# Kernel optimization log

Hardware: AMD Instinct MI355X
Metric: run time of the kernel (lower is better)

Reference implementation:

```python
import jax, jax.numpy as jnp
import numpy as np

SOS_TOKEN = 0


def setup_inputs() -> dict:
    key = jax.random.key(0)
    ks = jax.random.split(key, 16)
    B, S, T, H, V = 64, 64, 32, 512, 32000
    s = 1.0 / np.sqrt(H)
    inp = {
        "encoder_outputs": jax.random.normal(ks[0], (B, S, H), jnp.float32),
        "encoder_hidden": jax.random.normal(ks[1], (1, B, H), jnp.float32),
        "target_tensor": jax.random.randint(ks[2], (B, T), 0, V),
        "emb": jax.random.normal(ks[3], (V, H), jnp.float32),
        "Wa": jax.random.uniform(ks[4], (H, H), jnp.float32, -s, s),
        "ba": jnp.zeros((H,), jnp.float32),
        "Ua": jax.random.uniform(ks[5], (H, H), jnp.float32, -s, s),
        "bu": jnp.zeros((H,), jnp.float32),
        "va": jax.random.uniform(ks[6], (H, 1), jnp.float32, -s, s),
        "bv": jnp.zeros((1,), jnp.float32),
        "w_ih": jax.random.uniform(ks[7], (3 * H, 2 * H), jnp.float32, -s, s),
        "b_ih": jax.random.uniform(ks[8], (3 * H,), jnp.float32, -s, s),
        "w_hh": jax.random.uniform(ks[9], (3 * H, H), jnp.float32, -s, s),
        "b_hh": jax.random.uniform(ks[10], (3 * H,), jnp.float32, -s, s),
        "Wo": jax.random.uniform(ks[11], (V, H), jnp.float32, -s, s),
        "bo": jax.random.uniform(ks[12], (V,), jnp.float32, -s, s),
    }
    return inp


def _gru_cell(x, h, w_ih, b_ih, w_hh, b_hh):
    # x: [B, 2H], h: [B, H] -- PyTorch nn.GRU gate math
    H = h.shape[-1]
    gi = x @ w_ih.T + b_ih            # [B, 3H]
    gh = h @ w_hh.T + b_hh            # [B, 3H]
    i_r, i_z, i_n = gi[:, :H], gi[:, H:2 * H], gi[:, 2 * H:]
    h_r, h_z, h_n = gh[:, :H], gh[:, H:2 * H], gh[:, 2 * H:]
    r = jax.nn.sigmoid(i_r + h_r)
    z = jax.nn.sigmoid(i_z + h_z)
    n = jnp.tanh(i_n + r * h_n)
    return (1.0 - z) * n + z * h


def reference(encoder_outputs, encoder_hidden, target_tensor,
              emb, Wa, ba, Ua, bu, va, bv,
              w_ih, b_ih, w_hh, b_hh, Wo, bo):
    B, S, H = encoder_outputs.shape
    T = target_tensor.shape[1]
    # Teacher forcing: step t input is SOS for t=0 else target[:, t-1]
    sos = jnp.full((B, 1), SOS_TOKEN, dtype=target_tensor.dtype)
    input_ids = jnp.concatenate([sos, target_tensor[:, :-1]], axis=1)  # [B, T]
    embedded = emb[input_ids]  # [B, T, H]  (dropout is identity in eval)

    # Precompute key projection once (invariant across steps)
    Ua_keys = encoder_outputs @ Ua.T + bu  # [B, S, H]

    def step(h, x_emb):
        # Bahdanau additive attention: query = hidden state
        scores = jnp.tanh(h[:, None, :] @ Wa.T + ba + Ua_keys) @ va + bv  # [B, S, 1]
        scores = scores[..., 0]                                           # [B, S]
        attn = jax.nn.softmax(scores, axis=-1)
        context = jnp.einsum('bs,bsh->bh', attn, encoder_outputs)
        x = jnp.concatenate([x_emb, context], axis=-1)                    # [B, 2H]
        h_new = _gru_cell(x, h, w_ih, b_ih, w_hh, b_hh)
        logits = h_new @ Wo.T + bo                                        # [B, V]
        return h_new, (logits, attn)

    h0 = encoder_hidden[0]  # [B, H]
    h_final, (logits_t, attn_t) = jax.lax.scan(step, h0, jnp.swapaxes(embedded, 0, 1))
    logits = jnp.swapaxes(logits_t, 0, 1)        # [B, T, V]
    attentions = jnp.swapaxes(attn_t, 0, 1)      # [B, T, S]
    log_probs = jax.nn.log_softmax(logits, axis=-1)
    decoder_hidden = h_final[None]               # [1, B, H]
    return (log_probs, decoder_hidden, attentions)
```

## Files before the change

kernel.cpp:

```cpp
#include <hip/hip_runtime.h>

typedef unsigned short u16;
typedef __bf16 bf16x8 __attribute__((ext_vector_type(8)));
typedef float f32x4 __attribute__((ext_vector_type(4)));

#define Bsz 64
#define Ssz 64
#define Tsz 32
#define Hsz 512
#define Vsz 32000
#define NCONV 160
#define NTOT 256

#define MAIL_BG 0
#define MAIL_GB 2048
#define MAIL_GG 4096
#define NMAIL 5120

static __device__ inline u16 f2bf(float f) {
    union { float f; unsigned u; } v; v.f = f;
    unsigned u = v.u;
    unsigned r = (u + 0x7FFFu + ((u >> 16) & 1u)) >> 16;
    return (u16)r;
}
static __device__ inline float bf2f(u16 v) {
    union { unsigned u; float f; } x; x.u = ((unsigned)v) << 16; return x.f;
}
static __device__ inline float tanh_fast(float x) {
    float e = __expf(2.f * x);
    return 1.f - 2.f / (e + 1.f);
}
static __device__ inline void st_u32(unsigned* p, unsigned v) {
    __hip_atomic_store(p, v, __ATOMIC_RELAXED, __HIP_MEMORY_SCOPE_AGENT);
}
static __device__ inline unsigned ld_u32(const unsigned* p) {
    return __hip_atomic_load(p, __ATOMIC_RELAXED, __HIP_MEMORY_SCOPE_AGENT);
}

#define GLOAD_LDS16(g, l) \
    __builtin_amdgcn_global_load_lds((const __attribute__((address_space(1))) void*)(g), \
                                     (__attribute__((address_space(3))) void*)(l), 16, 0, 0)

__global__ void prep_kernel(const float* __restrict__ enc, const float* __restrict__ Ua,
                            const float* __restrict__ Wa, const float* __restrict__ wih,
                            const float* __restrict__ whh, const float* __restrict__ ehid,
                            const int* __restrict__ target, const float* __restrict__ emb,
                            u16* __restrict__ encbf, u16* __restrict__ Uabf,
                            u16* __restrict__ Wabf, u16* __restrict__ wihbf,
                            u16* __restrict__ whhbf, u16* __restrict__ h0bf,
                            u16* __restrict__ xbuf) {
    const int n0 = 2097152, n1 = 262144, n2 = 262144, n3 = 1572864, n4 = 786432, n5 = 32768;
    const int n6 = Tsz * Bsz * Hsz;
    const int total = n0 + n1 + n2 + n3 + n4 + n5 + n6;
    for (int i = blockIdx.x * blockDim.x + threadIdx.x; i < total; i += gridDim.x * blockDim.x) {
        int j = i;
        if (j < n0) { encbf[j] = f2bf(enc[j]); continue; } j -= n0;
        if (j < n1) { Uabf[j] = f2bf(Ua[j]); continue; } j -= n1;
        if (j < n2) { Wabf[j] = f2bf(Wa[j]); continue; } j -= n2;
        if (j < n3) { wihbf[j] = f2bf(wih[j]); continue; } j -= n3;
        if (j < n4) { whhbf[j] = f2bf(whh[j]); continue; } j -= n4;
        if (j < n5) { h0bf[j] = f2bf(ehid[j]); continue; } j -= n5;
        {
            int t = j / (Bsz * Hsz);
            int rem = j % (Bsz * Hsz);
            int b = rem / Hsz, k = rem % Hsz;
            int id = (t == 0) ? 0 : target[b * Tsz + (t - 1)];
            xbuf[((size_t)t * Bsz + b) * 1024 + k] = f2bf(emb[(size_t)id * Hsz + k]);
        }
    }
}

__global__ __launch_bounds__(256) void gemm_bt(const u16* __restrict__ A, const u16* __restrict__ Bw,
                                               const float* __restrict__ bias, float* __restrict__ out,
                                               int M, int N, int K) {
    __shared__ __align__(16) u16 As[128 * 32];
    __shared__ __align__(16) u16 Bs[128 * 32];
    int m0 = blockIdx.x * 128, n0 = blockIdx.y * 128;
    int tid = threadIdx.x, lane = tid & 63, wid = tid >> 6;
    int wm = wid & 1, wn = wid >> 1;
    f32x4 acc[4][4] = {};
    for (int k0 = 0; k0 < K; k0 += 32) {
        int e0 = wid * 64 + lane;
        int e1 = e0 + 256;
        GLOAD_LDS16(&A[(size_t)(m0 + (e0 >> 2)) * K + k0 + (e0 & 3) * 8], (char*)As + wid * 1024);
        GLOAD_LDS16(&A[(size_t)(m0 + (e1 >> 2)) * K + k0 + (e1 & 3) * 8], (char*)As + 4096 + wid * 1024);
        GLOAD_LDS16(&Bw[(size_t)(n0 + (e0 >> 2)) * K + k0 + (e0 & 3) * 8], (char*)Bs + wid * 1024);
        GLOAD_LDS16(&Bw[(size_t)(n0 + (e1 >> 2)) * K + k0 + (e1 & 3) * 8], (char*)Bs + 4096 + wid * 1024);
        __syncthreads();
        bf16x8 av[4], bvv[4];
        for (int mi = 0; mi < 4; ++mi)
            av[mi] = *(const bf16x8*)&As[(wm * 64 + mi * 16 + (lane & 15)) * 32 + (lane >> 4) * 8];
        for (int ni = 0; ni < 4; ++ni)
            bvv[ni] = *(const bf16x8*)&Bs[(wn * 64 + ni * 16 + (lane & 15)) * 32 + (lane >> 4) * 8];
        for (int mi = 0; mi < 4; ++mi)
            for (int ni = 0; ni < 4; ++ni)
                acc[mi][ni] = __builtin_amdgcn_mfma_f32_16x16x32_bf16(av[mi], bvv[ni], acc[mi][ni], 0, 0, 0);
        __syncthreads();
    }
    for (int mi = 0; mi < 4; ++mi)
        for (int ni = 0; ni < 4; ++ni) {
            int n = n0 + wn * 64 + ni * 16 + (lane & 15);
            float bb = bias[n];
            for (int r = 0; r < 4; ++r) {
                int m = m0 + wm * 64 + mi * 16 + (lane >> 4) * 4 + r;
                out[(size_t)m * N + n] = acc[mi][ni][r] + bb;
            }
        }
}

__global__ __launch_bounds__(512, 1) void coop_kernel(
    const float* __restrict__ uak,
    u16* __restrict__ xbuf, u16* __restrict__ Abf,
    const u16* __restrict__ h0bf, const u16* __restrict__ wihbf, const u16* __restrict__ whhbf,
    const u16* __restrict__ Wabf, const float* __restrict__ enc,
    const float* __restrict__ va, const float* __restrict__ bv, const float* __restrict__ ba,
    const float* __restrict__ b_ih, const float* __restrict__ b_hh,
    const float* __restrict__ ehid,
    const float* __restrict__ Wo, u16* __restrict__ Wobf,
    float* __restrict__ out, u16* __restrict__ partials,
    unsigned* __restrict__ bar) {
    __shared__ __align__(16) char lds[149504];
    __shared__ float WhL[512];
    __shared__ float scL[64];
    __shared__ float vaL[512];

    const size_t HID_OFF = (size_t)Bsz * Tsz * Vsz;
    const size_t ATT_OFF = HID_OFF + (size_t)Bsz * Hsz;

    int tid = threadIdx.x, lane = tid & 63, wid = tid >> 6;
    int ln15 = lane & 15, hi = lane >> 4;
    int bx = blockIdx.x;

    unsigned* xbufU = (unsigned*)xbuf;
    unsigned* AbfU = (unsigned*)Abf;
    unsigned* partU = (unsigned*)partials;

    if (bx < 64) {
        int b = bx;
        u16* uakL = (u16*)lds;
        u16* encL = (u16*)(lds + 65536);
        float* attL = (float*)(lds + 131072);
        for (int i = tid; i < Ssz * Hsz; i += 512) {
            uakL[i] = f2bf(uak[(size_t)b * Ssz * Hsz + i]);
            encL[i] = f2bf(enc[(size_t)b * Ssz * Hsz + i]);
        }
        vaL[tid] = va[tid];
        float bvv = bv[0];
        float ba_t = ba[tid];
        int halfsel = tid & 1;
        __syncthreads();

        for (int t = 0; t < Tsz; ++t) {
            if (tid < 32) {
                unsigned* p = &bar[(MAIL_GB + b * 32 + tid) * 32];
                while (ld_u32(p) < (unsigned)(t + 1)) asm volatile("s_sleep 1");
            }
            __syncthreads();
            {
                float acc = ba_t;
                const unsigned* pb = partU + (size_t)b * 256 + (tid >> 1);
#pragma unroll
                for (int g = 0; g < 32; ++g) {
                    unsigned pw = ld_u32(pb + (size_t)g * 16384);
                    acc += bf2f((u16)(halfsel ? (pw >> 16) : (pw & 0xffff)));
                }
                WhL[tid] = acc;
            }
            __syncthreads();
            for (int si = 0; si < 8; ++si) {
                int s = wid * 8 + si;
                float a = 0.f;
#pragma unroll
                for (int ji = 0; ji < 8; ++ji) {
                    int j = lane + ji * 64;
                    float x = WhL[j] + bf2f(uakL[s * 512 + j]);
                    a += tanh_fast(x) * vaL[j];
                }
                for (int off = 32; off; off >>= 1) a += __shfl_down(a, off);
                if (lane == 0) scL[s] = a + bvv;
            }
            __syncthreads();
            if (wid == 0) {
                float x = scL[lane];
                float mx = x;
                for (int off = 32; off; off >>= 1) mx = fmaxf(mx, __shfl_xor(mx, off));
                float e = __expf(x - mx);
                float sm = e;
                for (int off = 32; off; off >>= 1) sm += __shfl_xor(sm, off);
                float at = e / sm;
                scL[lane] = at;
                attL[t * 64 + lane] = at;
            }
            __syncthreads();
            float c = 0.f;
            for (int s = 0; s < Ssz; ++s)
                c += scL[s] * bf2f(encL[s * 512 + tid]);
            unsigned me = (unsigned)f2bf(c);
            unsigned other = __shfl_xor(me, 1);
            if ((tid & 1) == 0)
                st_u32(&xbufU[((size_t)t * Bsz + b) * 512 + 256 + (tid >> 1)], me | (other << 16));
            asm volatile("s_waitcnt vmcnt(0)" ::: "memory");
            __syncthreads();
            if (tid < 32) st_u32(&bar[(MAIL_BG + tid * 64 + b) * 32], (unsigned)(t + 1));
        }
        __syncthreads();
        for (int i = tid; i < Tsz * Ssz; i += 512)
            out[ATT_OFF + (size_t)b * (Tsz * Ssz) + i] = attL[i];
    } else if (bx < 96) {
        int g = bx - 64, jbase = g * 16;
        u16* hsl = (u16*)(lds + 147456);
        for (int i = tid; i < 6144; i += 512) {
            int row = i >> 7, c16 = i & 127;
            int Rg = (row >> 4) * 512 + jbase + (row & 15);
            uint4 v = *(const uint4*)&wihbf[(size_t)Rg * 1024 + c16 * 8];
            *(uint4*)(lds + row * 2048 + ((c16 * 16) ^ ((row & 7) << 4))) = v;
        }
        for (int i = tid; i < 3072; i += 512) {
            int row = i >> 6, c16 = i & 63;
            int Rg = (row >> 4) * 512 + jbase + (row & 15);
            uint4 v = *(const uint4*)&whhbf[(size_t)Rg * 512 + c16 * 8];
            *(uint4*)(lds + 98304 + row * 1024 + ((c16 * 16) ^ ((row & 7) << 4))) = v;
        }
        const char* wih_l = lds;
        const char* whh_l = lds + 98304;
        int j = jbase + ln15;
        float bir = b_ih[j] + b_hh[j];
        float biz = b_ih[512 + j] + b_hh[512 + j];
        float bin = b_ih[1024 + j];
        float bhn = b_hh[1024 + j];
        float hp0 = 0.f, hp1 = 0.f, hp2 = 0.f, hp3 = 0.f;
        if (wid < 4) {
            int m = wid;
            hp0 = ehid[(size_t)(m * 16 + hi * 4 + 0) * Hsz + j];
            hp1 = ehid[(size_t)(m * 16 + hi * 4 + 1) * Hsz + j];
            hp2 = ehid[(size_t)(m * 16 + hi * 4 + 2) * Hsz + j];
            hp3 = ehid[(size_t)(m * 16 + hi * 4 + 3) * Hsz + j];
        }
        int swz = (ln15 & 7) << 4;
        bf16x8 zfr = {};
        bf16x8 wfrag[4];
#pragma unroll
        for (int i = 0; i < 4; ++i) {
            int jp = (wid * 4 + i) * 16 + ln15;
            wfrag[i] = (hi < 2) ? *(const bf16x8*)&Wabf[(size_t)jp * 512 + jbase + hi * 8] : zfr;
        }
        for (int i = tid; i < 1024; i += 512)
            hsl[i] = h0bf[(size_t)(i >> 4) * 512 + jbase + (i & 15)];
        __syncthreads();
#pragma unroll
        for (int mt = 0; mt < 4; ++mt) {
            bf16x8 af = (hi < 2) ? *(const bf16x8*)&hsl[(mt * 16 + ln15) * 16 + hi * 8] : zfr;
#pragma unroll
            for (int i = 0; i < 4; ++i) {
                f32x4 pacc = {};
                pacc = __builtin_amdgcn_mfma_f32_16x16x32_bf16(af, wfrag[i], pacc, 0, 0, 0);
                int n0 = (wid * 4 + i) * 16;
#pragma unroll
                for (int r = 0; r < 4; ++r) {
                    int b = mt * 16 + hi * 4 + r;
                    unsigned me = (unsigned)f2bf(pacc[r]);
                    unsigned other = __shfl_xor(me, 1);
                    if ((ln15 & 1) == 0)
                        st_u32(&partU[((size_t)g * 64 + b) * 256 + ((n0 + ln15) >> 1)], me | (other << 16));
                }
            }
        }
        asm volatile("s_waitcnt vmcnt(0)" ::: "memory");
        __syncthreads();
        if (tid < 64) st_u32(&bar[(MAIL_GB + tid * 32 + g) * 32], 1u);
        else if (tid < 96) st_u32(&bar[(MAIL_GG + (tid - 64) * 32 + g) * 32], 1u);

        for (int t = 0; t < Tsz; ++t) {
            const u16* hbt = t ? (Abf + (size_t)(t - 1) * Bsz * Hsz) : h0bf;
            f32x4 ar = {}, az = {}, ain = {}, ahn = {};
            if (wid < 4) {
                int m = wid;
#pragma unroll 8
                for (int k0 = 0; k0 < 16; ++k0) {
                    bf16x8 a = *(const bf16x8*)&xbuf[((size_t)t * Bsz + m * 16 + ln15) * 1024 + k0 * 32 + hi * 8];
                    int byteIn = k0 * 64 + hi * 16;
                    bf16x8 b0 = *(const bf16x8*)(wih_l + (0 + ln15) * 2048 + (byteIn ^ swz));
                    bf16x8 b1 = *(const bf16x8*)(wih_l + (16 + ln15) * 2048 + (byteIn ^ swz));
                    bf16x8 b2 = *(const bf16x8*)(wih_l + (32 + ln15) * 2048 + (byteIn ^ swz));
                    ar = __builtin_amdgcn_mfma_f32_16x16x32_bf16(a, b0, ar, 0, 0, 0);
                    az = __builtin_amdgcn_mfma_f32_16x16x32_bf16(a, b1, az, 0, 0, 0);
                    ain = __builtin_amdgcn_mfma_f32_16x16x32_bf16(a, b2, ain, 0, 0, 0);
                }
            }
            if (tid < 32) {
                unsigned* p = &bar[(MAIL_GG + g * 32 + tid) * 32];
                while (ld_u32(p) < (unsigned)(t + 1)) asm volatile("s_sleep 1");
            }
            __syncthreads();
            if (wid < 4) {
                int m = wid;
#pragma unroll 8
                for (int k0 = 0; k0 < 16; ++k0) {
                    bf16x8 a = *(const bf16x8*)&hbt[(size_t)(m * 16 + ln15) * 512 + k0 * 32 + hi * 8];
                    int byteIn = k0 * 64 + hi * 16;
                    bf16x8 b0 = *(const bf16x8*)(whh_l + (0 + ln15) * 1024 + (byteIn ^ swz));
                    bf16x8 b1 = *(const bf16x8*)(whh_l + (16 + ln15) * 1024 + (byteIn ^ swz));
                    bf16x8 b2 = *(const bf16x8*)(whh_l + (32 + ln15) * 1024 + (byteIn ^ swz));
                    ar = __builtin_amdgcn_mfma_f32_16x16x32_bf16(a, b0, ar, 0, 0, 0);
                    az = __builtin_amdgcn_mfma_f32_16x16x32_bf16(a, b1, az, 0, 0, 0);
                    ahn = __builtin_amdgcn_mfma_f32_16x16x32_bf16(a, b2, ahn, 0, 0, 0);
                }
                unsigned* p = &bar[(MAIL_BG + g * 64 + wid * 16 + ln15) * 32];
                while (ld_u32(p) < (unsigned)(t + 1)) asm volatile("s_sleep 1");
#pragma unroll 8
                for (int k0 = 16; k0 < 32; ++k0) {
                    bf16x8 a = *(const bf16x8*)&xbuf[((size_t)t * Bsz + m * 16 + ln15) * 1024 + k0 * 32 + hi * 8];
                    int byteIn = k0 * 64 + hi * 16;
                    bf16x8 b0 = *(const bf16x8*)(wih_l + (0 + ln15) * 2048 + (byteIn ^ swz));
                    bf16x8 b1 = *(const bf16x8*)(wih_l + (16 + ln15) * 2048 + (byteIn ^ swz));
                    bf16x8 b2 = *(const bf16x8*)(wih_l + (32 + ln15) * 2048 + (byteIn ^ swz));
                    ar = __builtin_amdgcn_mfma_f32_16x16x32_bf16(a, b0, ar, 0, 0, 0);
                    az = __builtin_amdgcn_mfma_f32_16x16x32_bf16(a, b1, az, 0, 0, 0);
                    ain = __builtin_amdgcn_mfma_f32_16x16x32_bf16(a, b2, ain, 0, 0, 0);
                }
                float hpv[4] = {hp0, hp1, hp2, hp3};
#pragma unroll
                for (int r = 0; r < 4; ++r) {
                    int b = m * 16 + hi * 4 + r;
                    float rg = 1.f / (1.f + __expf(-(ar[r] + bir)));
                    float zg = 1.f / (1.f + __expf(-(az[r] + biz)));
                    float ng = tanh_fast(ain[r] + bin + rg * (ahn[r] + bhn));
                    float hv = (1.f - zg) * ng + zg * hpv[r];
                    hpv[r] = hv;
                    u16 hb = f2bf(hv);
                    unsigned me = (unsigned)hb;
                    unsigned other = __shfl_xor(me, 1);
                    if ((ln15 & 1) == 0)
                        st_u32(&AbfU[((size_t)t * Bsz + b) * 256 + (j >> 1)], me | (other << 16));
                    hsl[b * 16 + ln15] = hb;
                    if (t == Tsz - 1) out[HID_OFF + (size_t)b * 512 + j] = hv;
                }
                hp0 = hpv[0]; hp1 = hpv[1]; hp2 = hpv[2]; hp3 = hpv[3];
            }
            __syncthreads();
#pragma unroll
            for (int mt = 0; mt < 4; ++mt) {
                bf16x8 af = (hi < 2) ? *(const bf16x8*)&hsl[(mt * 16 + ln15) * 16 + hi * 8] : zfr;
#pragma unroll
                for (int i = 0; i < 4; ++i) {
                    f32x4 pacc = {};
                    pacc = __builtin_amdgcn_mfma_f32_16x16x32_bf16(af, wfrag[i], pacc, 0, 0, 0);
                    int n0 = (wid * 4 + i) * 16;
#pragma unroll
                    for (int r = 0; r < 4; ++r) {
                        int b = mt * 16 + hi * 4 + r;
                        unsigned me = (unsigned)f2bf(pacc[r]);
                        unsigned other = __shfl_xor(me, 1);
                        if ((ln15 & 1) == 0)
                            st_u32(&partU[((size_t)g * 64 + b) * 256 + ((n0 + ln15) >> 1)], me | (other << 16));
                    }
                }
            }
            asm volatile("s_waitcnt vmcnt(0)" ::: "memory");
            __syncthreads();
            if (tid < 64) st_u32(&bar[(MAIL_GB + tid * 32 + g) * 32], (unsigned)(t + 2));
            else if (tid < 96) st_u32(&bar[(MAIL_GG + (tid - 64) * 32 + g) * 32], (unsigned)(t + 2));
        }
    } else {
        const float4* W4 = (const float4*)Wo;
        for (int i = (bx - 96) * 512 + tid; i < (Vsz * Hsz) / 4; i += NCONV * 512) {
            float4 v = W4[i];
            ushort4 o;
            o.x = f2bf(v.x); o.y = f2bf(v.y); o.z = f2bf(v.z); o.w = f2bf(v.w);
            *(ushort4*)&Wobf[(size_t)i * 4] = o;
        }
    }
}

template <int BF16OUT>
__global__ __launch_bounds__(512) void gemm_logits(const u16* __restrict__ Abf, const u16* __restrict__ Wobf,
                                                   const float* __restrict__ bo, float* __restrict__ out,
                                                   u16* __restrict__ scr, float* __restrict__ sumexp) {
    __shared__ __align__(16) char lds[49152];
    char* As0 = lds;
    char* Bs0 = lds + 8192;
    char* As1 = lds + 24576;
    char* Bs1 = lds + 32768;
    int tid = threadIdx.x, lane = tid & 63, wid = tid >> 6;
    int ln15 = lane & 15, hi = lane >> 4;
    int wm = wid & 1, wn = wid >> 1;
    int job = blockIdx.x;
    int m0 = (job / 125) * 128, n0 = (job % 125) * 256;
    f32x4 acc[4][4] = {};
    {
        int e0 = wid * 64 + lane, r = e0 >> 2, c8 = (e0 & 3) * 8;
        GLOAD_LDS16(&Abf[(size_t)(m0 + r) * 512 + c8], As0 + wid * 1024);
        GLOAD_LDS16(&Wobf[(size_t)(n0 + r) * 512 + c8], Bs0 + wid * 1024);
        GLOAD_LDS16(&Wobf[(size_t)(n0 + 128 + r) * 512 + c8], Bs0 + 8192 + wid * 1024);
    }
#pragma unroll 2
    for (int ks = 0; ks < 16; ++ks) {
        const u16* As = (const u16*)((ks & 1) ? As1 : As0);
        const u16* Bs = (const u16*)((ks & 1) ? Bs1 : Bs0);
        if (ks < 15) {
            char* Asn = (ks & 1) ? As0 : As1;
            char* Bsn = (ks & 1) ? Bs0 : Bs1;
            int e0 = wid * 64 + lane, r = e0 >> 2, c8 = (e0 & 3) * 8;
            int k0 = (ks + 1) * 32;
            GLOAD_LDS16(&Abf[(size_t)(m0 + r) * 512 + k0 + c8], Asn + wid * 1024);
            GLOAD_LDS16(&Wobf[(size_t)(n0 + r) * 512 + k0 + c8], Bsn + wid * 1024);
            GLOAD_LDS16(&Wobf[(size_t)(n0 + 128 + r) * 512 + k0 + c8], Bsn + 8192 + wid * 1024);
            asm volatile("s_waitcnt vmcnt(3)" ::: "memory");
        } else {
            asm volatile("s_waitcnt vmcnt(0)" ::: "memory");
        }
        __builtin_amdgcn_s_barrier();
        bf16x8 av[4], bvv[4];
        for (int mi = 0; mi < 4; ++mi)
            av[mi] = *(const bf16x8*)&As[(wm * 64 + mi * 16 + ln15) * 32 + hi * 8];
        for (int ni = 0; ni < 4; ++ni)
            bvv[ni] = *(const bf16x8*)&Bs[(wn * 64 + ni * 16 + ln15) * 32 + hi * 8];
        for (int mi = 0; mi < 4; ++mi)
            for (int ni = 0; ni < 4; ++ni)
                acc[mi][ni] = __builtin_amdgcn_mfma_f32_16x16x32_bf16(av[mi], bvv[ni], acc[mi][ni], 0, 0, 0);
        asm volatile("s_waitcnt lgkmcnt(0)" ::: "memory");
        __builtin_amdgcn_s_barrier();
    }
    float* eps = (float*)lds;
    float bb[4];
#pragma unroll
    for (int ni = 0; ni < 4; ++ni) bb[ni] = bo[n0 + wn * 64 + ni * 16 + ln15];
    for (int mi = 0; mi < 4; ++mi) {
        __syncthreads();
#pragma unroll
        for (int ni = 0; ni < 4; ++ni)
#pragma unroll
            for (int r = 0; r < 4; ++r)
                eps[(wm * 16 + hi * 4 + r) * 256 + wn * 64 + ni * 16 + ln15] = acc[mi][ni][r] + bb[ni];
        __syncthreads();
#pragma unroll
        for (int k = 0; k < 4; ++k) {
            int idx = k * 512 + tid;
            int l = idx >> 6, c4 = idx & 63;
            int m = m0 + (l >> 4) * 64 + mi * 16 + (l & 15);
            int t = m >> 6, b = m & 63;
            float4 v = *(float4*)&eps[l * 256 + c4 * 4];
            if (BF16OUT) {
                ushort4 o;
                o.x = f2bf(v.x); o.y = f2bf(v.y); o.z = f2bf(v.z); o.w = f2bf(v.w);
                *(ushort4*)&scr[((size_t)(b * Tsz + t)) * Vsz + n0 + c4 * 4] = o;
            } else {
                *(float4*)&out[((size_t)(b * Tsz + t)) * Vsz + n0 + c4 * 4] = v;
            }
            float e = __expf(v.x) + __expf(v.y) + __expf(v.z) + __expf(v.w);
            for (int off = 32; off; off >>= 1) e += __shfl_down(e, off);
            if (lane == 0) atomicAdd(&sumexp[(m & 63) * Tsz + (m >> 6)], e);
        }
    }
}

__global__ void sub_kernel(float* __restrict__ out, const float* __restrict__ sumexp) {
    const int total4 = (Bsz * Tsz * Vsz) / 4;
    float4* o4 = (float4*)out;
    for (int i = blockIdx.x * blockDim.x + threadIdx.x; i < total4; i += gridDim.x * blockDim.x) {
        float l = __logf(sumexp[i / (Vsz / 4)]);
        float4 v = o4[i];
        v.x -= l; v.y -= l; v.z -= l; v.w -= l;
        o4[i] = v;
    }
}

__global__ void sub_bf16_kernel(const u16* __restrict__ scr, const float* __restrict__ sumexp,
                                float* __restrict__ out) {
    const int total8 = (Bsz * Tsz * Vsz) / 8;
    for (int i = blockIdx.x * blockDim.x + threadIdx.x; i < total8; i += gridDim.x * blockDim.x) {
        float l = __logf(sumexp[i / (Vsz / 8)]);
        uint4 v = *(const uint4*)&scr[(size_t)i * 8];
        float4 a, b;
        a.x = bf2f((u16)v.x) - l;        a.y = bf2f((u16)(v.x >> 16)) - l;
        a.z = bf2f((u16)v.y) - l;        a.w = bf2f((u16)(v.y >> 16)) - l;
        b.x = bf2f((u16)v.z) - l;        b.y = bf2f((u16)(v.z >> 16)) - l;
        b.z = bf2f((u16)v.w) - l;        b.w = bf2f((u16)(v.w >> 16)) - l;
        *(float4*)&out[(size_t)i * 8] = a;
        *(float4*)&out[(size_t)i * 8 + 4] = b;
    }
}

extern "C" void kernel_launch(void* const* d_in, const int* in_sizes, int n_in,
                              void* d_out, int out_size, void* d_ws, size_t ws_size,
                              hipStream_t stream) {
    const float* enc   = (const float*)d_in[0];
    const float* ehid  = (const float*)d_in[1];
    const int*   target= (const int*)d_in[2];
    const float* emb   = (const float*)d_in[3];
    const float* Wa    = (const float*)d_in[4];
    const float* ba    = (const float*)d_in[5];
    const float* Ua    = (const float*)d_in[6];
    const float* bu    = (const float*)d_in[7];
    const float* va    = (const float*)d_in[8];
    const float* bv    = (const float*)d_in[9];
    const float* w_ih  = (const float*)d_in[10];
    const float* b_ih  = (const float*)d_in[11];
    const float* w_hh  = (const float*)d_in[12];
    const float* b_hh  = (const float*)d_in[13];
    const float* Wo    = (const float*)d_in[14];
    const float* bo    = (const float*)d_in[15];
    float* out = (float*)d_out;

    char* w = (char*)d_ws;
    float* uak    = (float*)w; w += (size_t)4096 * 512 * 4;
    float* sumexp = (float*)w; w += 8192;
    unsigned* bar = (unsigned*)w; w += (size_t)NMAIL * 128;
    u16* xbuf     = (u16*)w;   w += (size_t)Tsz * Bsz * 1024 * 2;
    u16* Abf      = (u16*)w;   w += (size_t)Tsz * Bsz * Hsz * 2;
    u16* h0bf     = (u16*)w;   w += (size_t)Bsz * Hsz * 2;
    u16* partials = (u16*)w;   w += (size_t)32 * Bsz * Hsz * 2;
    u16* Wabf     = (u16*)w;   w += (size_t)Hsz * Hsz * 2;
    u16* encbf    = (u16*)w;   w += (size_t)4096 * 512 * 2;
    u16* Uabf     = (u16*)w;   w += (size_t)Hsz * Hsz * 2;
    u16* wihbf    = (u16*)w;   w += (size_t)1536 * 1024 * 2;
    u16* whhbf    = (u16*)w;   w += (size_t)1536 * 512 * 2;
    u16* Wobf     = (u16*)w;   w += (size_t)Vsz * 512 * 2;
    u16* scrbf    = (u16*)w;   w += (size_t)Bsz * Tsz * Vsz * 2;
    const int use_bf16 = (ws_size >= (size_t)(w - (char*)d_ws));

    prep_kernel<<<2048, 256, 0, stream>>>(enc, Ua, Wa, w_ih, w_hh, ehid, target, emb,
                                          encbf, Uabf, Wabf, wihbf, whhbf, h0bf, xbuf);

    gemm_bt<<<dim3(32, 4), 256, 0, stream>>>(encbf, Uabf, bu, uak, 4096, 512, 512);

    hipMemsetAsync(bar, 0, (size_t)NMAIL * 128, stream);
    hipMemsetAsync(sumexp, 0, 2048 * 4, stream);

    coop_kernel<<<NTOT, 512, 0, stream>>>(uak, xbuf, Abf, h0bf, wihbf, whhbf,
                                          Wabf, enc, va, bv, ba, b_ih, b_hh,
                                          ehid, Wo, Wobf, out, partials, bar);

    if (use_bf16) {
        gemm_logits<1><<<2000, 512, 0, stream>>>(Abf, Wobf, bo, out, scrbf, sumexp);
        sub_bf16_kernel<<<4096, 256, 0, stream>>>(scrbf, sumexp, out);
    } else {
        gemm_logits<0><<<2000, 512, 0, stream>>>(Abf, Wobf, bo, out, scrbf, sumexp);
        sub_kernel<<<2048, 256, 0, stream>>>(out, sumexp);
    }
}
```

Baseline: 819.3 us.

## Fuse key projection GEMM and weight bf16 conversion into cooperative kernel

Removes the separate gemm_bt launch and fp32 uak round trip by computing the Ua key projection per batch inside the attention blocks with MFMA from LDS-resident encoder data. The GRU blocks now convert w_ih/w_hh from fp32 to bf16 while loading into LDS, so the prep kernel no longer converts encoder outputs or GRU weights. This cuts launches and global traffic but adds serial work at the start of the persistent kernel, reading Ua fragments straight from global memory.

Result: no change. 819.7 us (+0.1%).

```diff
diff --git a/kernel.cpp b/kernel.cpp
--- a/kernel.cpp
+++ b/kernel.cpp
@@ -36,29 +36,31 @@
 static __device__ inline unsigned ld_u32(const unsigned* p) {
     return __hip_atomic_load(p, __ATOMIC_RELAXED, __HIP_MEMORY_SCOPE_AGENT);
 }
+static __device__ inline uint4 pack8(float4 a, float4 b) {
+    uint4 o;
+    o.x = (unsigned)f2bf(a.x) | ((unsigned)f2bf(a.y) << 16);
+    o.y = (unsigned)f2bf(a.z) | ((unsigned)f2bf(a.w) << 16);
+    o.z = (unsigned)f2bf(b.x) | ((unsigned)f2bf(b.y) << 16);
+    o.w = (unsigned)f2bf(b.z) | ((unsigned)f2bf(b.w) << 16);
+    return o;
+}
 
 #define GLOAD_LDS16(g, l) \
     __builtin_amdgcn_global_load_lds((const __attribute__((address_space(1))) void*)(g), \
                                      (__attribute__((address_space(3))) void*)(l), 16, 0, 0)
 
-__global__ void prep_kernel(const float* __restrict__ enc, const float* __restrict__ Ua,
-                            const float* __restrict__ Wa, const float* __restrict__ wih,
-                            const float* __restrict__ whh, const float* __restrict__ ehid,
+__global__ void prep_kernel(const float* __restrict__ Ua, const float* __restrict__ Wa,
+                            const float* __restrict__ ehid,
                             const int* __restrict__ target, const float* __restrict__ emb,
-                            u16* __restrict__ encbf, u16* __restrict__ Uabf,
-                            u16* __restrict__ Wabf, u16* __restrict__ wihbf,
-                            u16* __restrict__ whhbf, u16* __restrict__ h0bf,
-                            u16* __restrict__ xbuf) {
-    const int n0 = 2097152, n1 = 262144, n2 = 262144, n3 = 1572864, n4 = 786432, n5 = 32768;
+                            u16* __restrict__ Uabf, u16* __restrict__ Wabf,
+                            u16* __restrict__ h0bf, u16* __restrict__ xbuf) {
+    const int n1 = 262144, n2 = 262144, n5 = 32768;
     const int n6 = Tsz * Bsz * Hsz;
-    const int total = n0 + n1 + n2 + n3 + n4 + n5 + n6;
+    const int total = n1 + n2 + n5 + n6;
     for (int i = blockIdx.x * blockDim.x + threadIdx.x; i < total; i += gridDim.x * blockDim.x) {
         int j = i;
-        if (j < n0) { encbf[j] = f2bf(enc[j]); continue; } j -= n0;
         if (j < n1) { Uabf[j] = f2bf(Ua[j]); continue; } j -= n1;
         if (j < n2) { Wabf[j] = f2bf(Wa[j]); continue; } j -= n2;
-        if (j < n3) { wihbf[j] = f2bf(wih[j]); continue; } j -= n3;
-        if (j < n4) { whhbf[j] = f2bf(whh[j]); continue; } j -= n4;
         if (j < n5) { h0bf[j] = f2bf(ehid[j]); continue; } j -= n5;
         {
             int t = j / (Bsz * Hsz);
@@ -70,48 +72,10 @@
     }
 }
 
-__global__ __launch_bounds__(256) void gemm_bt(const u16* __restrict__ A, const u16* __restrict__ Bw,
-                                               const float* __restrict__ bias, float* __restrict__ out,
-                                               int M, int N, int K) {
-    __shared__ __align__(16) u16 As[128 * 32];
-    __shared__ __align__(16) u16 Bs[128 * 32];
-    int m0 = blockIdx.x * 128, n0 = blockIdx.y * 128;
-    int tid = threadIdx.x, lane = tid & 63, wid = tid >> 6;
-    int wm = wid & 1, wn = wid >> 1;
-    f32x4 acc[4][4] = {};
-    for (int k0 = 0; k0 < K; k0 += 32) {
-        int e0 = wid * 64 + lane;
-        int e1 = e0 + 256;
-        GLOAD_LDS16(&A[(size_t)(m0 + (e0 >> 2)) * K + k0 + (e0 & 3) * 8], (char*)As + wid * 1024);
-        GLOAD_LDS16(&A[(size_t)(m0 + (e1 >> 2)) * K + k0 + (e1 & 3) * 8], (char*)As + 4096 + wid * 1024);
-        GLOAD_LDS16(&Bw[(size_t)(n0 + (e0 >> 2)) * K + k0 + (e0 & 3) * 8], (char*)Bs + wid * 1024);
-        GLOAD_LDS16(&Bw[(size_t)(n0 + (e1 >> 2)) * K + k0 + (e1 & 3) * 8], (char*)Bs + 4096 + wid * 1024);
-        __syncthreads();
-        bf16x8 av[4], bvv[4];
-        for (int mi = 0; mi < 4; ++mi)
-            av[mi] = *(const bf16x8*)&As[(wm * 64 + mi * 16 + (lane & 15)) * 32 + (lane >> 4) * 8];
-        for (int ni = 0; ni < 4; ++ni)
-            bvv[ni] = *(const bf16x8*)&Bs[(wn * 64 + ni * 16 + (lane & 15)) * 32 + (lane >> 4) * 8];
-        for (int mi = 0; mi < 4; ++mi)
-            for (int ni = 0; ni < 4; ++ni)
-                acc[mi][ni] = __builtin_amdgcn_mfma_f32_16x16x32_bf16(av[mi], bvv[ni], acc[mi][ni], 0, 0, 0);
-        __syncthreads();
-    }
-    for (int mi = 0; mi < 4; ++mi)
-        for (int ni = 0; ni < 4; ++ni) {
-            int n = n0 + wn * 64 + ni * 16 + (lane & 15);
-            float bb = bias[n];
-            for (int r = 0; r < 4; ++r) {
-                int m = m0 + wm * 64 + mi * 16 + (lane >> 4) * 4 + r;
-                out[(size_t)m * N + n] = acc[mi][ni][r] + bb;
-            }
-        }
-}
-
 __global__ __launch_bounds__(512, 1) void coop_kernel(
-    const float* __restrict__ uak,
     u16* __restrict__ xbuf, u16* __restrict__ Abf,
-    const u16* __restrict__ h0bf, const u16* __restrict__ wihbf, const u16* __restrict__ whhbf,
+    const u16* __restrict__ h0bf, const u16* __restrict__ Uabf, const float* __restrict__ bu,
+    const float* __restrict__ wih, const float* __restrict__ whh,
     const u16* __restrict__ Wabf, const float* __restrict__ enc,
     const float* __restrict__ va, const float* __restrict__ bv, const float* __restrict__ ba,
     const float* __restrict__ b_ih, const float* __restrict__ b_hh,
@@ -140,14 +104,41 @@
         u16* uakL = (u16*)lds;
         u16* encL = (u16*)(lds + 65536);
         float* attL = (float*)(lds + 131072);
-        for (int i = tid; i < Ssz * Hsz; i += 512) {
-            uakL[i] = f2bf(uak[(size_t)b * Ssz * Hsz + i]);
+        for (int i = tid; i < Ssz * Hsz; i += 512)
             encL[i] = f2bf(enc[(size_t)b * Ssz * Hsz + i]);
-        }
         vaL[tid] = va[tid];
         float bvv = bv[0];
         float ba_t = ba[tid];
         int halfsel = tid & 1;
+        __syncthreads();
+        {
+            f32x4 ua[4][4] = {};
+#pragma unroll
+            for (int k0 = 0; k0 < 16; ++k0) {
+                bf16x8 af[4], bfr[4];
+#pragma unroll
+                for (int mt = 0; mt < 4; ++mt)
+                    af[mt] = *(const bf16x8*)&encL[(mt * 16 + ln15) * 512 + k0 * 32 + hi * 8];
+#pragma unroll
+                for (int jt = 0; jt < 4; ++jt)
+                    bfr[jt] = *(const bf16x8*)&Uabf[(size_t)(wid * 64 + jt * 16 + ln15) * 512 + k0 * 32 + hi * 8];
+#pragma unroll
+                for (int mt = 0; mt < 4; ++mt)
+#pragma unroll
+                    for (int jt = 0; jt < 4; ++jt)
+                        ua[mt][jt] = __builtin_amdgcn_mfma_f32_16x16x32_bf16(af[mt], bfr[jt], ua[mt][jt], 0, 0, 0);
+            }
+#pragma unroll
+            for (int mt = 0; mt < 4; ++mt)
+#pragma unroll
+                for (int jt = 0; jt < 4; ++jt) {
+                    int jj = wid * 64 + jt * 16 + ln15;
+                    float bj = bu[jj];
+#pragma unroll
+                    for (int r = 0; r < 4; ++r)
+                        uakL[(mt * 16 + hi * 4 + r) * 512 + jj] = f2bf(ua[mt][jt][r] + bj);
+                }
+        }
         __syncthreads();
 
         for (int t = 0; t < Tsz; ++t) {
@@ -212,14 +203,18 @@
         for (int i = tid; i < 6144; i += 512) {
             int row = i >> 7, c16 = i & 127;
             int Rg = (row >> 4) * 512 + jbase + (row & 15);
-            uint4 v = *(const uint4*)&wihbf[(size_t)Rg * 1024 + c16 * 8];
-            *(uint4*)(lds + row * 2048 + ((c16 * 16) ^ ((row & 7) << 4))) = v;
+            const float* src = &wih[(size_t)Rg * 1024 + c16 * 8];
+            float4 v0 = *(const float4*)src;
+            float4 v1 = *(const float4*)(src + 4);
+            *(uint4*)(lds + row * 2048 + ((c16 * 16) ^ ((row & 7) << 4))) = pack8(v0, v1);
         }
         for (int i = tid; i < 3072; i += 512) {
             int row = i >> 6, c16 = i & 63;
             int Rg = (row >> 4) * 512 + jbase + (row & 15);
-            uint4 v = *(const uint4*)&whhbf[(size_t)Rg * 512 + c16 * 8];
-            *(uint4*)(lds + 98304 + row * 1024 + ((c16 * 16) ^ ((row & 7) << 4))) = v;
+            const float* src = &whh[(size_t)Rg * 512 + c16 * 8];
+            float4 v0 = *(const float4*)src;
+            float4 v1 = *(const float4*)(src + 4);
+            *(uint4*)(lds + 98304 + row * 1024 + ((c16 * 16) ^ ((row & 7) << 4))) = pack8(v0, v1);
         }
         const char* wih_l = lds;
         const char* whh_l = lds + 98304;
@@ -503,7 +498,6 @@
     float* out = (float*)d_out;
 
     char* w = (char*)d_ws;
-    float* uak    = (float*)w; w += (size_t)4096 * 512 * 4;
     float* sumexp = (float*)w; w += 8192;
     unsigned* bar = (unsigned*)w; w += (size_t)NMAIL * 128;
     u16* xbuf     = (u16*)w;   w += (size_t)Tsz * Bsz * 1024 * 2;
@@ -511,23 +505,17 @@
     u16* h0bf     = (u16*)w;   w += (size_t)Bsz * Hsz * 2;
     u16* partials = (u16*)w;   w += (size_t)32 * Bsz * Hsz * 2;
     u16* Wabf     = (u16*)w;   w += (size_t)Hsz * Hsz * 2;
-    u16* encbf    = (u16*)w;   w += (size_t)4096 * 512 * 2;
     u16* Uabf     = (u16*)w;   w += (size_t)Hsz * Hsz * 2;
-    u16* wihbf    = (u16*)w;   w += (size_t)1536 * 1024 * 2;
-    u16* whhbf    = (u16*)w;   w += (size_t)1536 * 512 * 2;
     u16* Wobf     = (u16*)w;   w += (size_t)Vsz * 512 * 2;
     u16* scrbf    = (u16*)w;   w += (size_t)Bsz * Tsz * Vsz * 2;
     const int use_bf16 = (ws_size >= (size_t)(w - (char*)d_ws));
 
-    prep_kernel<<<2048, 256, 0, stream>>>(enc, Ua, Wa, w_ih, w_hh, ehid, target, emb,
-                                          encbf, Uabf, Wabf, wihbf, whhbf, h0bf, xbuf);
-
-    gemm_bt<<<dim3(32, 4), 256, 0, stream>>>(encbf, Uabf, bu, uak, 4096, 512, 512);
+    prep_kernel<<<512, 256, 0, stream>>>(Ua, Wa, ehid, target, emb, Uabf, Wabf, h0bf, xbuf);
 
     hipMemsetAsync(bar, 0, (size_t)NMAIL * 128, stream);
     hipMemsetAsync(sumexp, 0, 2048 * 4, stream);
 
-    coop_kernel<<<NTOT, 512, 0, stream>>>(uak, xbuf, Abf, h0bf, wihbf, whhbf,
+    coop_kernel<<<NTOT, 512, 0, stream>>>(xbuf, Abf, h0bf, Uabf, bu, w_ih, w_hh,
                                           Wabf, enc, va, bv, ba, b_ih, b_hh,
                                           ehid, Wo, Wobf, out, partials, bar);
 
```

## Compute full query projection in dedicated waves and simplify mailbox synchronisation

Applied to the files above, without the earlier changes.

The old code had GRU blocks compute 16-wide K-slices of h@Wa.T and write 32 partial sums, which attention blocks then reduced. Now waves 4-7 of each GRU block compute full-K output tiles of h@Wa.T for their 16 columns, reading h from global memory. They write one bf16 result per step and signal per-wave flags, so attention blocks do a single load instead of a 32-way reduction. GRU waves no longer need a block-wide barrier and signal per wave; wih/whh are converted to bf16 inside the coop kernel instead of in prep. The cost is a longer query-projection step (16 MFMAs over the full K) sitting on the critical path of the recurrence, plus per-step global reads of h.

Measured after the change: 835.3 us. Within noise of the previous version (+2.0%).

```diff
diff --git a/kernel.cpp b/kernel.cpp
--- a/kernel.cpp
+++ b/kernel.cpp
@@ -12,10 +12,9 @@
 #define NCONV 160
 #define NTOT 256
 
-#define MAIL_BG 0
-#define MAIL_GB 2048
-#define MAIL_GG 4096
-#define NMAIL 5120
+#define FW_BASE 128
+#define FC_BASE 256
+#define NSLOT 320
 
 static __device__ inline u16 f2bf(float f) {
     union { float f; unsigned u; } v; v.f = f;
@@ -36,29 +35,33 @@
 static __device__ inline unsigned ld_u32(const unsigned* p) {
     return __hip_atomic_load(p, __ATOMIC_RELAXED, __HIP_MEMORY_SCOPE_AGENT);
 }
+static __device__ inline uint4 pack8(float4 a, float4 b) {
+    uint4 o;
+    o.x = (unsigned)f2bf(a.x) | ((unsigned)f2bf(a.y) << 16);
+    o.y = (unsigned)f2bf(a.z) | ((unsigned)f2bf(a.w) << 16);
+    o.z = (unsigned)f2bf(b.x) | ((unsigned)f2bf(b.y) << 16);
+    o.w = (unsigned)f2bf(b.z) | ((unsigned)f2bf(b.w) << 16);
+    return o;
+}
 
 #define GLOAD_LDS16(g, l) \
     __builtin_amdgcn_global_load_lds((const __attribute__((address_space(1))) void*)(g), \
                                      (__attribute__((address_space(3))) void*)(l), 16, 0, 0)
 
 __global__ void prep_kernel(const float* __restrict__ enc, const float* __restrict__ Ua,
-                            const float* __restrict__ Wa, const float* __restrict__ wih,
-                            const float* __restrict__ whh, const float* __restrict__ ehid,
+                            const float* __restrict__ Wa, const float* __restrict__ ehid,
                             const int* __restrict__ target, const float* __restrict__ emb,
                             u16* __restrict__ encbf, u16* __restrict__ Uabf,
-                            u16* __restrict__ Wabf, u16* __restrict__ wihbf,
-                            u16* __restrict__ whhbf, u16* __restrict__ h0bf,
+                            u16* __restrict__ Wabf, u16* __restrict__ h0bf,
                             u16* __restrict__ xbuf) {
-    const int n0 = 2097152, n1 = 262144, n2 = 262144, n3 = 1572864, n4 = 786432, n5 = 32768;
+    const int n0 = 2097152, n1 = 262144, n2 = 262144, n5 = 32768;
     const int n6 = Tsz * Bsz * Hsz;
-    const int total = n0 + n1 + n2 + n3 + n4 + n5 + n6;
+    const int total = n0 + n1 + n2 + n5 + n6;
     for (int i = blockIdx.x * blockDim.x + threadIdx.x; i < total; i += gridDim.x * blockDim.x) {
         int j = i;
         if (j < n0) { encbf[j] = f2bf(enc[j]); continue; } j -= n0;
         if (j < n1) { Uabf[j] = f2bf(Ua[j]); continue; } j -= n1;
         if (j < n2) { Wabf[j] = f2bf(Wa[j]); continue; } j -= n2;
-        if (j < n3) { wihbf[j] = f2bf(wih[j]); continue; } j -= n3;
-        if (j < n4) { whhbf[j] = f2bf(whh[j]); continue; } j -= n4;
         if (j < n5) { h0bf[j] = f2bf(ehid[j]); continue; } j -= n5;
         {
             int t = j / (Bsz * Hsz);
@@ -111,15 +114,16 @@
 __global__ __launch_bounds__(512, 1) void coop_kernel(
     const float* __restrict__ uak,
     u16* __restrict__ xbuf, u16* __restrict__ Abf,
-    const u16* __restrict__ h0bf, const u16* __restrict__ wihbf, const u16* __restrict__ whhbf,
+    const u16* __restrict__ h0bf,
+    const float* __restrict__ wih, const float* __restrict__ whh,
     const u16* __restrict__ Wabf, const float* __restrict__ enc,
     const float* __restrict__ va, const float* __restrict__ bv, const float* __restrict__ ba,
     const float* __restrict__ b_ih, const float* __restrict__ b_hh,
     const float* __restrict__ ehid,
     const float* __restrict__ Wo, u16* __restrict__ Wobf,
-    float* __restrict__ out, u16* __restrict__ partials,
+    float* __restrict__ out, unsigned* __restrict__ WhbU,
     unsigned* __restrict__ bar) {
-    __shared__ __align__(16) char lds[149504];
+    __shared__ __align__(16) char lds[147456];
     __shared__ float WhL[512];
     __shared__ float scL[64];
     __shared__ float vaL[512];
@@ -133,10 +137,10 @@
 
     unsigned* xbufU = (unsigned*)xbuf;
     unsigned* AbfU = (unsigned*)Abf;
-    unsigned* partU = (unsigned*)partials;
 
     if (bx < 64) {
         int b = bx;
+        int mtile = b >> 4;
         u16* uakL = (u16*)lds;
         u16* encL = (u16*)(lds + 65536);
         float* attL = (float*)(lds + 131072);
@@ -152,19 +156,13 @@
 
         for (int t = 0; t < Tsz; ++t) {
             if (tid < 32) {
-                unsigned* p = &bar[(MAIL_GB + b * 32 + tid) * 32];
+                unsigned* p = &bar[(FW_BASE + tid * 4 + mtile) * 32];
                 while (ld_u32(p) < (unsigned)(t + 1)) asm volatile("s_sleep 1");
             }
             __syncthreads();
             {
-                float acc = ba_t;
-                const unsigned* pb = partU + (size_t)b * 256 + (tid >> 1);
-#pragma unroll
-                for (int g = 0; g < 32; ++g) {
-                    unsigned pw = ld_u32(pb + (size_t)g * 16384);
-                    acc += bf2f((u16)(halfsel ? (pw >> 16) : (pw & 0xffff)));
-                }
-                WhL[tid] = acc;
+                unsigned pw = ld_u32(&WhbU[(size_t)t * 16384 + b * 256 + (tid >> 1)]);
+                WhL[tid] = bf2f((u16)(halfsel ? (pw >> 16) : (pw & 0xffff))) + ba_t;
             }
             __syncthreads();
             for (int si = 0; si < 8; ++si) {
@@ -201,80 +199,78 @@
                 st_u32(&xbufU[((size_t)t * Bsz + b) * 512 + 256 + (tid >> 1)], me | (other << 16));
             asm volatile("s_waitcnt vmcnt(0)" ::: "memory");
             __syncthreads();
-            if (tid < 32) st_u32(&bar[(MAIL_BG + tid * 64 + b) * 32], (unsigned)(t + 1));
+            if (tid == 0) st_u32(&bar[(FC_BASE + b) * 32], (unsigned)(t + 1));
         }
         __syncthreads();
         for (int i = tid; i < Tsz * Ssz; i += 512)
             out[ATT_OFF + (size_t)b * (Tsz * Ssz) + i] = attL[i];
     } else if (bx < 96) {
         int g = bx - 64, jbase = g * 16;
-        u16* hsl = (u16*)(lds + 147456);
         for (int i = tid; i < 6144; i += 512) {
             int row = i >> 7, c16 = i & 127;
             int Rg = (row >> 4) * 512 + jbase + (row & 15);
-            uint4 v = *(const uint4*)&wihbf[(size_t)Rg * 1024 + c16 * 8];
-            *(uint4*)(lds + row * 2048 + ((c16 * 16) ^ ((row & 7) << 4))) = v;
+            const float* src = &wih[(size_t)Rg * 1024 + c16 * 8];
+            float4 v0 = *(const float4*)src;
+            float4 v1 = *(const float4*)(src + 4);
+            *(uint4*)(lds + row * 2048 + ((c16 * 16) ^ ((row & 7) << 4))) = pack8(v0, v1);
         }
         for (int i = tid; i < 3072; i += 512) {
             int row = i >> 6, c16 = i & 63;
             int Rg = (row >> 4) * 512 + jbase + (row & 15);
-            uint4 v = *(const uint4*)&whhbf[(size_t)Rg * 512 + c16 * 8];
-            *(uint4*)(lds + 98304 + row * 1024 + ((c16 * 16) ^ ((row & 7) << 4))) = v;
-        }
-        const char* wih_l = lds;
-        const char* whh_l = lds + 98304;
-        int j = jbase + ln15;
-        float bir = b_ih[j] + b_hh[j];
-        float biz = b_ih[512 + j] + b_hh[512 + j];
-        float bin = b_ih[1024 + j];
-        float bhn = b_hh[1024 + j];
-        float hp0 = 0.f, hp1 = 0.f, hp2 = 0.f, hp3 = 0.f;
-        if (wid < 4) {
-            int m = wid;
-            hp0 = ehid[(size_t)(m * 16 + hi * 4 + 0) * Hsz + j];
-            hp1 = ehid[(size_t)(m * 16 + hi * 4 + 1) * Hsz + j];
-            hp2 = ehid[(size_t)(m * 16 + hi * 4 + 2) * Hsz + j];
-            hp3 = ehid[(size_t)(m * 16 + hi * 4 + 3) * Hsz + j];
-        }
-        int swz = (ln15 & 7) << 4;
-        bf16x8 zfr = {};
-        bf16x8 wfrag[4];
-#pragma unroll
-        for (int i = 0; i < 4; ++i) {
-            int jp = (wid * 4 + i) * 16 + ln15;
-            wfrag[i] = (hi < 2) ? *(const bf16x8*)&Wabf[(size_t)jp * 512 + jbase + hi * 8] : zfr;
-        }
-        for (int i = tid; i < 1024; i += 512)
-            hsl[i] = h0bf[(size_t)(i >> 4) * 512 + jbase + (i & 15)];
-        __syncthreads();
-#pragma unroll
-        for (int mt = 0; mt < 4; ++mt) {
-            bf16x8 af = (hi < 2) ? *(const bf16x8*)&hsl[(mt * 16 + ln15) * 16 + hi * 8] : zfr;
-#pragma unroll
-            for (int i = 0; i < 4; ++i) {
-                f32x4 pacc = {};
-                pacc = __builtin_amdgcn_mfma_f32_16x16x32_bf16(af, wfrag[i], pacc, 0, 0, 0);
-                int n0 = (wid * 4 + i) * 16;
+            const float* src = &whh[(size_t)Rg * 512 + c16 * 8];
+            float4 v0 = *(const float4*)src;
+            float4 v1 = *(const float4*)(src + 4);
+            *(uint4*)(lds + 98304 + row * 1024 + ((c16 * 16) ^ ((row & 7) << 4))) = pack8(v0, v1);
+        }
+        __syncthreads();
+
+        if (wid >= 4) {
+            int i = wid - 4;
+            bf16x8 wfragW[16];
+#pragma unroll
+            for (int k0 = 0; k0 < 16; ++k0)
+                wfragW[k0] = *(const bf16x8*)&Wabf[(size_t)(jbase + ln15) * 512 + k0 * 32 + hi * 8];
+            for (int t = 0; t < Tsz; ++t) {
+                const u16* hbt = t ? (Abf + (size_t)(t - 1) * Bsz * Hsz) : h0bf;
+                if (t) {
+                    unsigned* p = &bar[((lane & 31) * 4 + i) * 32];
+                    while (ld_u32(p) < (unsigned)t) asm volatile("s_sleep 1");
+                }
+                f32x4 accW = {};
+#pragma unroll
+                for (int k0 = 0; k0 < 16; ++k0) {
+                    bf16x8 a = *(const bf16x8*)&hbt[(size_t)(i * 16 + ln15) * 512 + k0 * 32 + hi * 8];
+                    accW = __builtin_amdgcn_mfma_f32_16x16x32_bf16(a, wfragW[k0], accW, 0, 0, 0);
+                }
+                unsigned* WhT = WhbU + (size_t)t * 16384;
 #pragma unroll
                 for (int r = 0; r < 4; ++r) {
-                    int b = mt * 16 + hi * 4 + r;
-                    unsigned me = (unsigned)f2bf(pacc[r]);
+                    unsigned me = (unsigned)f2bf(accW[r]);
                     unsigned other = __shfl_xor(me, 1);
                     if ((ln15 & 1) == 0)
-                        st_u32(&partU[((size_t)g * 64 + b) * 256 + ((n0 + ln15) >> 1)], me | (other << 16));
-                }
-            }
-        }
-        asm volatile("s_waitcnt vmcnt(0)" ::: "memory");
-        __syncthreads();
-        if (tid < 64) st_u32(&bar[(MAIL_GB + tid * 32 + g) * 32], 1u);
-        else if (tid < 96) st_u32(&bar[(MAIL_GG + (tid - 64) * 32 + g) * 32], 1u);
-
-        for (int t = 0; t < Tsz; ++t) {
-            const u16* hbt = t ? (Abf + (size_t)(t - 1) * Bsz * Hsz) : h0bf;
-            f32x4 ar = {}, az = {}, ain = {}, ahn = {};
-            if (wid < 4) {
-                int m = wid;
+                        st_u32(&WhT[(i * 16 + hi * 4 + r) * 256 + ((jbase + ln15) >> 1)], me | (other << 16));
+                }
+                asm volatile("s_waitcnt vmcnt(0)" ::: "memory");
+                if (lane == 0) st_u32(&bar[(FW_BASE + g * 4 + i) * 32], (unsigned)(t + 1));
+            }
+        } else {
+            int m = wid;
+            const char* wih_l = lds;
+            const char* whh_l = lds + 98304;
+            int j = jbase + ln15;
+            float bir = b_ih[j] + b_hh[j];
+            float biz = b_ih[512 + j] + b_hh[512 + j];
+            float bin = b_ih[1024 + j];
+            float bhn = b_hh[1024 + j];
+            float hp0 = ehid[(size_t)(m * 16 + hi * 4 + 0) * Hsz + j];
+            float hp1 = ehid[(size_t)(m * 16 + hi * 4 + 1) * Hsz + j];
+            float hp2 = ehid[(size_t)(m * 16 + hi * 4 + 2) * Hsz + j];
+            float hp3 = ehid[(size_t)(m * 16 + hi * 4 + 3) * Hsz + j];
+            int swz = (ln15 & 7) << 4;
+
+            for (int t = 0; t < Tsz; ++t) {
+                const u16* hbt = t ? (Abf + (size_t)(t - 1) * Bsz * Hsz) : h0bf;
+                f32x4 ar = {}, az = {}, ain = {}, ahn = {};
 #pragma unroll 8
                 for (int k0 = 0; k0 < 16; ++k0) {
                     bf16x8 a = *(const bf16x8*)&xbuf[((size_t)t * Bsz + m * 16 + ln15) * 1024 + k0 * 32 + hi * 8];
@@ -286,14 +282,10 @@
                     az = __builtin_amdgcn_mfma_f32_16x16x32_bf16(a, b1, az, 0, 0, 0);
                     ain = __builtin_amdgcn_mfma_f32_16x16x32_bf16(a, b2, ain, 0, 0, 0);
                 }
-            }
-            if (tid < 32) {
-                unsigned* p = &bar[(MAIL_GG + g * 32 + tid) * 32];
-                while (ld_u32(p) < (unsigned)(t + 1)) asm volatile("s_sleep 1");
-            }
-            __syncthreads();
-            if (wid < 4) {
-                int m = wid;
+                if (t) {
+                    unsigned* p = &bar[((lane & 31) * 4 + m) * 32];
+                    while (ld_u32(p) < (unsigned)t) asm volatile("s_sleep 1");
+                }
 #pragma unroll 8
                 for (int k0 = 0; k0 < 16; ++k0) {
                     bf16x8 a = *(const bf16x8*)&hbt[(size_t)(m * 16 + ln15) * 512 + k0 * 32 + hi * 8];
@@ -305,8 +297,10 @@
                     az = __builtin_amdgcn_mfma_f32_16x16x32_bf16(a, b1, az, 0, 0, 0);
                     ahn = __builtin_amdgcn_mfma_f32_16x16x32_bf16(a, b2, ahn, 0, 0, 0);
                 }
-                unsigned* p = &bar[(MAIL_BG + g * 64 + wid * 16 + ln15) * 32];
-                while (ld_u32(p) < (unsigned)(t + 1)) asm volatile("s_sleep 1");
+                {
+                    unsigned* p = &bar[(FC_BASE + m * 16 + ln15) * 32];
+                    while (ld_u32(p) < (unsigned)(t + 1)) asm volatile("s_sleep 1");
+                }
 #pragma unroll 8
                 for (int k0 = 16; k0 < 32; ++k0) {
                     bf16x8 a = *(const bf16x8*)&xbuf[((size_t)t * Bsz + m * 16 + ln15) * 1024 + k0 * 32 + hi * 8];
@@ -327,39 +321,16 @@
                     float ng = tanh_fast(ain[r] + bin + rg * (ahn[r] + bhn));
                     float hv = (1.f - zg) * ng + zg * hpv[r];
                     hpv[r] = hv;
-                    u16 hb = f2bf(hv);
-                    unsigned me = (unsigned)hb;
+                    unsigned me = (unsigned)f2bf(hv);
                     unsigned other = __shfl_xor(me, 1);
                     if ((ln15 & 1) == 0)
                         st_u32(&AbfU[((size_t)t * Bsz + b) * 256 + (j >> 1)], me | (other << 16));
-                    hsl[b * 16 + ln15] = hb;
                     if (t == Tsz - 1) out[HID_OFF + (size_t)b * 512 + j] = hv;
                 }
                 hp0 = hpv[0]; hp1 = hpv[1]; hp2 = hpv[2]; hp3 = hpv[3];
-            }
-            __syncthreads();
-#pragma unroll
-            for (int mt = 0; mt < 4; ++mt) {
-                bf16x8 af = (hi < 2) ? *(const bf16x8*)&hsl[(mt * 16 + ln15) * 16 + hi * 8] : zfr;
-#pragma unroll
-                for (int i = 0; i < 4; ++i) {
-                    f32x4 pacc = {};
-                    pacc = __builtin_amdgcn_mfma_f32_16x16x32_bf16(af, wfrag[i], pacc, 0, 0, 0);
-                    int n0 = (wid * 4 + i) * 16;
-#pragma unroll
-                    for (int r = 0; r < 4; ++r) {
-                        int b = mt * 16 + hi * 4 + r;
-                        unsigned me = (unsigned)f2bf(pacc[r]);
-                        unsigned other = __shfl_xor(me, 1);
-                        if ((ln15 & 1) == 0)
-                            st_u32(&partU[((size_t)g * 64 + b) * 256 + ((n0 + ln15) >> 1)], me | (other << 16));
-                    }
-                }
-            }
-            asm volatile("s_waitcnt vmcnt(0)" ::: "memory");
-            __syncthreads();
-            if (tid < 64) st_u32(&bar[(MAIL_GB + tid * 32 + g) * 32], (unsigned)(t + 2));
-            else if (tid < 96) st_u32(&bar[(MAIL_GG + (tid - 64) * 32 + g) * 32], (unsigned)(t + 2));
+                asm volatile("s_waitcnt vmcnt(0)" ::: "memory");
+                if (lane == 0) st_u32(&bar[(g * 4 + m) * 32], (unsigned)(t + 1));
+            }
         }
     } else {
         const float4* W4 = (const float4*)Wo;
@@ -505,31 +476,29 @@
     char* w = (char*)d_ws;
     float* uak    = (float*)w; w += (size_t)4096 * 512 * 4;
     float* sumexp = (float*)w; w += 8192;
-    unsigned* bar = (unsigned*)w; w += (size_t)NMAIL * 128;
+    unsigned* bar = (unsigned*)w; w += (size_t)NSLOT * 128;
+    unsigned* WhbU= (unsigned*)w; w += (size_t)Tsz * Bsz * 256 * 4;
     u16* xbuf     = (u16*)w;   w += (size_t)Tsz * Bsz * 1024 * 2;
     u16* Abf      = (u16*)w;   w += (size_t)Tsz * Bsz * Hsz * 2;
     u16* h0bf     = (u16*)w;   w += (size_t)Bsz * Hsz * 2;
-    u16* partials = (u16*)w;   w += (size_t)32 * Bsz * Hsz * 2;
     u16* Wabf     = (u16*)w;   w += (size_t)Hsz * Hsz * 2;
     u16* encbf    = (u16*)w;   w += (size_t)4096 * 512 * 2;
     u16* Uabf     = (u16*)w;   w += (size_t)Hsz * Hsz * 2;
-    u16* wihbf    = (u16*)w;   w += (size_t)1536 * 1024 * 2;
-    u16* whhbf    = (u16*)w;   w += (size_t)1536 * 512 * 2;
     u16* Wobf     = (u16*)w;   w += (size_t)Vsz * 512 * 2;
     u16* scrbf    = (u16*)w;   w += (size_t)Bsz * Tsz * Vsz * 2;
     const int use_bf16 = (ws_size >= (size_t)(w - (char*)d_ws));
 
-    prep_kernel<<<2048, 256, 0, stream>>>(enc, Ua, Wa, w_ih, w_hh, ehid, target, emb,
-                                          encbf, Uabf, Wabf, wihbf, whhbf, h0bf, xbuf);
+    prep_kernel<<<1024, 256, 0, stream>>>(enc, Ua, Wa, ehid, target, emb,
+                                          encbf, Uabf, Wabf, h0bf, xbuf);
 
     gemm_bt<<<dim3(32, 4), 256, 0, stream>>>(encbf, Uabf, bu, uak, 4096, 512, 512);
 
-    hipMemsetAsync(bar, 0, (size_t)NMAIL * 128, stream);
+    hipMemsetAsync(bar, 0, (size_t)NSLOT * 128, stream);
     hipMemsetAsync(sumexp, 0, 2048 * 4, stream);
 
-    coop_kernel<<<NTOT, 512, 0, stream>>>(uak, xbuf, Abf, h0bf, wihbf, whhbf,
+    coop_kernel<<<NTOT, 512, 0, stream>>>(uak, xbuf, Abf, h0bf, w_ih, w_hh,
                                           Wabf, enc, va, bv, ba, b_ih, b_hh,
-                                          ehid, Wo, Wobf, out, partials, bar);
+                                          ehid, Wo, Wobf, out, WhbU, bar);
 
     if (use_bf16) {
         gemm_logits<1><<<2000, 512, 0, stream>>>(Abf, Wobf, bo, out, scrbf, sumexp);
```
